# Kernel tuning notes

Hardware: AMD Instinct MI355X
Metric: run time of the kernel (lower is better)

Reference implementation:

```python
import math
import jax, jax.numpy as jnp
import numpy as np

SQ = 5  # locality window width (static, from init_kwargs)

def _locality_mask_np(hidden_size: int, width: int) -> np.ndarray:
    """[H, H] 0/1 mask: units live on a side x side grid; unit i connects to
    unit j iff their circular (wrap-around) Chebyshev grid distance <= width//2.
    mask_type='circular' -> toroidal wrap."""
    side = int(round(math.sqrt(hidden_size)))
    assert side * side == hidden_size
    r = np.arange(hidden_size) // side
    c = np.arange(hidden_size) % side
    dr = np.abs(r[:, None] - r[None, :])
    dc = np.abs(c[:, None] - c[None, :])
    dr = np.minimum(dr, side - dr)  # circular wrap
    dc = np.minimum(dc, side - dc)
    half = width // 2
    return ((dr <= half) & (dc <= half)).astype(np.float32)


def setup_inputs() -> dict:
    key = jax.random.key(0)
    ks = jax.random.split(key, 8)
    B, S, H = 8, 2048, 1024
    scale = 0.02
    x = jax.random.normal(ks[0], (B, S, H), dtype=jnp.float32)
    Wq = jax.random.normal(ks[1], (H, H), dtype=jnp.float32) * scale
    Wk = jax.random.normal(ks[2], (H, H), dtype=jnp.float32) * scale
    Wv = jax.random.normal(ks[3], (H, H), dtype=jnp.float32) * scale
    bq = jnp.zeros((H,), dtype=jnp.float32)
    bk = jnp.zeros((H,), dtype=jnp.float32)
    bv = jnp.zeros((H,), dtype=jnp.float32)
    Wl = jax.random.normal(ks[4], (H, H), dtype=jnp.float32) * scale
    return {"x": x, "Wq": Wq, "bq": bq, "Wk": Wk, "bk": bk,
            "Wv": Wv, "bv": bv, "Wl": Wl}


def reference(x, Wq, bq, Wk, bk, Wv, bv, Wl):
    H = x.shape[-1]
    mask = jnp.asarray(_locality_mask_np(H, SQ))  # [H, H], static
    # Locally-connected q/k/v projections: dense weight elementwise-masked.
    q = x @ (Wq * mask).T + bq  # [B, S, H]
    k = x @ (Wk * mask).T + bk
    v = x @ (Wv * mask).T + bv
    # Learned spatial querying: locality-masked learned map applied to query.
    q = q @ (Wl * mask).T  # [B, S, H]
    # Manual attention (dropout is identity in eval / p=0).
    scores = jnp.einsum("bsh,bth->bst", q, k) / math.sqrt(H)  # [B, S, S]
    probs = jax.nn.softmax(scores, axis=-1)
    out = jnp.einsum("bst,bth->bsh", probs, v)  # [B, S, H]
    return out, probs
```

## Files before the change

kernel.cpp:

```cpp
#include <hip/hip_runtime.h>

typedef __attribute__((ext_vector_type(8))) short short8;
typedef __attribute__((ext_vector_type(4))) float floatx4;

__device__ __forceinline__ unsigned short f2bf(float f) {
  union { float f; unsigned int u; } x; x.f = f;
  unsigned int r = (x.u + 0x7fffu + ((x.u >> 16) & 1u)) >> 16;
  return (unsigned short)r;
}
__device__ __forceinline__ float bf2f(unsigned short u) {
  union { unsigned int u; float f; } x; x.u = ((unsigned int)u) << 16;
  return x.f;
}

__device__ __forceinline__ void gload_lds16(const void* g, void* l) {
  __builtin_amdgcn_global_load_lds((const __attribute__((address_space(1))) void*)g,
                                   (__attribute__((address_space(3))) void*)l,
                                   16, 0, 0);
}

__global__ __launch_bounds__(128) void prep_weights(
    const float* __restrict__ Wq, const float* __restrict__ Wk,
    const float* __restrict__ Wv, const float* __restrict__ Wl,
    const float* __restrict__ bq, const float* __restrict__ bk,
    const float* __restrict__ bv,
    unsigned short* __restrict__ Wqkv, float* __restrict__ biasAll) {
  const int i = blockIdx.x;
  const int r = i >> 5, c = i & 31;
  const int t = threadIdx.x;
  {
    short8 z = (short8){0, 0, 0, 0, 0, 0, 0, 0};
    ((short8*)Wqkv)[i * 128 + t] = z;
    ((short8*)Wqkv)[(1024 + i) * 128 + t] = z;
    ((short8*)Wqkv)[(2048 + i) * 128 + t] = z;
  }
  __syncthreads();
  if (t < 25) {
    int dr = t / 5 - 2, dc = t % 5 - 2;
    int j = (((r + dr) & 31) << 5) | ((c + dc) & 31);
    Wqkv[(1024 + i) * 1024 + j] = f2bf(Wk[i * 1024 + j]);
    Wqkv[(2048 + i) * 1024 + j] = f2bf(Wv[i * 1024 + j]);
  }
  if (t < 81) {
    int dr = t / 9 - 4, dc = t % 9 - 4;
    int j = (((r + dr) & 31) << 5) | ((c + dc) & 31);
    float s = 0.f;
    int erlo = dr - 2 < -2 ? -2 : dr - 2, erhi = dr + 2 > 2 ? 2 : dr + 2;
    int eclo = dc - 2 < -2 ? -2 : dc - 2, echi = dc + 2 > 2 ? 2 : dc + 2;
    for (int er = erlo; er <= erhi; ++er)
      for (int ec = eclo; ec <= echi; ++ec) {
        int m = (((r + er) & 31) << 5) | ((c + ec) & 31);
        s += Wl[i * 1024 + m] * Wq[m * 1024 + j];
      }
    Wqkv[i * 1024 + j] = f2bf(s);
  }
  if (t == 96) {
    float s = 0.f;
    for (int e = 0; e < 25; ++e) {
      int dr = e / 5 - 2, dc = e % 5 - 2;
      int m = (((r + dr) & 31) << 5) | ((c + dc) & 31);
      s += Wl[i * 1024 + m] * bq[m];
    }
    biasAll[i] = s;
  }
  if (t == 97) biasAll[1024 + i] = bk[i];
  if (t == 98) biasAll[2048 + i] = bv[i];
}

__global__ __launch_bounds__(256) void cast_bf16(const float4* __restrict__ x,
                                                 ushort4* __restrict__ xb) {
  int i = blockIdx.x * 256 + threadIdx.x;
  float4 v = x[i];
  ushort4 o;
  o.x = f2bf(v.x); o.y = f2bf(v.y); o.z = f2bf(v.z); o.w = f2bf(v.w);
  xb[i] = o;
}

template <int OUTMODE>
__global__ __launch_bounds__(512, 2) void gemm256(
    const unsigned short* __restrict__ A, const unsigned short* __restrict__ B,
    void* __restrict__ Cv, const float* __restrict__ auxc, float* __restrict__ auxw,
    int lda, int ldb, int ldc, int K, float scale,
    size_t sA, size_t sB, size_t sC, int nx, int ny) {
  __shared__ __align__(16) unsigned short lds[67584];
  const int t = threadIdx.x;
  const int lane = t & 63;
  const int wv = t >> 6;
  const int wm = wv >> 2;
  const int wn = wv & 3;
  const int l15 = lane & 15, lq = lane >> 4;

  const int nwg = gridDim.x;
  const int hid = blockIdx.x;
  const int logical = (hid & 7) * (nwg >> 3) + (hid >> 3);
  const int bn = logical % nx;
  const int bm = (logical / nx) % ny;
  const int bz = logical / (nx * ny);

  A += sA * bz; B += sB * bz;

  const int srow = t >> 3;
  const int sg = (t & 7) ^ (srow & 7);

#define STG_A(h, tile_) do {                                                     \
    gload_lds16(A + (size_t)(bm * 256 + (h) * 128 + srow) * lda + (tile_) * 64 + sg * 8, \
                &lds[(((tile_) & 1) << 14) + (h) * 8192 + wv * 512]);            \
    gload_lds16(A + (size_t)(bm * 256 + (h) * 128 + 64 + srow) * lda + (tile_) * 64 + sg * 8, \
                &lds[(((tile_) & 1) << 14) + (h) * 8192 + 4096 + wv * 512]);     \
  } while (0)
#define STG_B(h, tile_) do {                                                     \
    gload_lds16(B + (size_t)(bn * 256 + (h) * 128 + srow) * ldb + (tile_) * 64 + sg * 8, \
                &lds[32768 + (((tile_) & 1) << 14) + (h) * 8192 + wv * 512]);    \
    gload_lds16(B + (size_t)(bn * 256 + (h) * 128 + 64 + srow) * ldb + (tile_) * 64 + sg * 8, \
                &lds[32768 + (((tile_) & 1) << 14) + (h) * 8192 + 4096 + wv * 512]); \
  } while (0)

#define LOADA(arr, ro)                                                           \
  _Pragma("unroll") for (int i = 0; i < 4; ++i) {                                \
    int rA = wm * 128 + (ro) + i * 16 + l15;                                     \
    _Pragma("unroll") for (int ks = 0; ks < 2; ++ks)                             \
      arr[i][ks] = *(const short8*)&lds[bo_ + rA * 64 + (((ks * 4 + lq) ^ (rA & 7)) << 3)]; \
  }
#define LOADB(arr, ro)                                                           \
  _Pragma("unroll") for (int j = 0; j < 2; ++j) {                                \
    int rB = wn * 64 + (ro) + j * 16 + l15;                                      \
    _Pragma("unroll") for (int ks = 0; ks < 2; ++ks)                             \
      arr[j][ks] = *(const short8*)&lds[32768 + bo_ + rB * 64 + (((ks * 4 + lq) ^ (rB & 7)) << 3)]; \
  }
#define MFMA8(mb, nb, aa, bb)                                                    \
  _Pragma("unroll") for (int i = 0; i < 4; ++i)                                  \
    _Pragma("unroll") for (int j = 0; j < 2; ++j) {                              \
      acc[(mb) + i][(nb) + j] = __builtin_amdgcn_mfma_f32_16x16x32_bf16(         \
          aa[i][0], bb[j][0], acc[(mb) + i][(nb) + j], 0, 0, 0);                 \
      acc[(mb) + i][(nb) + j] = __builtin_amdgcn_mfma_f32_16x16x32_bf16(         \
          aa[i][1], bb[j][1], acc[(mb) + i][(nb) + j], 0, 0, 0);                 \
    }
#define FENCE asm volatile("" ::: "memory")
#define BAR __builtin_amdgcn_s_barrier()
#define SP1 __builtin_amdgcn_s_setprio(1)
#define SP0 __builtin_amdgcn_s_setprio(0)

  floatx4 acc[8][4];
#pragma unroll
  for (int i = 0; i < 8; ++i)
#pragma unroll
    for (int j = 0; j < 4; ++j) acc[i][j] = (floatx4){0.f, 0.f, 0.f, 0.f};

  const int NT = K >> 6;

  STG_A(0, 0); STG_A(1, 0); STG_B(0, 0); STG_B(1, 0);
  FENCE;
  STG_B(0, 1); STG_A(0, 1); STG_B(1, 1);
  asm volatile("s_waitcnt vmcnt(6)" ::: "memory");
  BAR;

  for (int T = 0; T < NT; T += 2) {
    short8 aF[4][2], bFa[2][2], bFb[2][2];
    {
      const int bo_ = 0;
      LOADA(aF, 0); LOADB(bFa, 0);
      STG_A(1, T + 1);
      FENCE; BAR;
      SP1; MFMA8(0, 0, aF, bFa); SP0;
      FENCE; BAR;
      LOADB(bFb, 32);
      FENCE; BAR;
      SP1; MFMA8(0, 2, aF, bFb); SP0;
      FENCE; BAR;
      LOADA(aF, 64);
      if (T + 2 < NT) STG_B(0, T + 2);
      FENCE; BAR;
      SP1; MFMA8(4, 2, aF, bFb); SP0;
      FENCE; BAR;
      if (T + 2 < NT) STG_A(0, T + 2);
      FENCE; BAR;
      SP1; MFMA8(4, 0, aF, bFa); SP0;
      if (T + 2 < NT) { asm volatile("s_waitcnt vmcnt(4)" ::: "memory"); }
      else            { asm volatile("s_waitcnt vmcnt(0)" ::: "memory"); }
      FENCE; BAR;
    }
    {
      const int bo_ = 1 << 14;
      LOADA(aF, 0); LOADB(bFa, 0);
      if (T + 2 < NT) { STG_B(1, T + 2); STG_A(1, T + 2); }
      FENCE; BAR;
      SP1; MFMA8(0, 0, aF, bFa); SP0;
      FENCE; BAR;
      LOADB(bFb, 32);
      FENCE; BAR;
      SP1; MFMA8(0, 2, aF, bFb); SP0;
      FENCE; BAR;
      LOADA(aF, 64);
      if (T + 3 < NT) STG_B(0, T + 3);
      FENCE; BAR;
      SP1; MFMA8(4, 2, aF, bFb); SP0;
      FENCE; BAR;
      if (T + 3 < NT) { STG_A(0, T + 3); STG_B(1, T + 3); }
      FENCE; BAR;
      SP1; MFMA8(4, 0, aF, bFa); SP0;
      if (T + 3 < NT) { asm volatile("s_waitcnt vmcnt(6)" ::: "memory"); }
      else            { asm volatile("s_waitcnt vmcnt(0)" ::: "memory"); }
      FENCE; BAR;
    }
  }
#undef STG_A
#undef STG_B
#undef LOADA
#undef LOADB
#undef MFMA8

  const int row0 = bm * 256 + wm * 128;
  const int col0 = bn * 256 + wn * 64;

  if (OUTMODE == 0) {
    if (bn < 8) {
      unsigned short* C = (unsigned short*)Cv;
#pragma unroll
      for (int m = 0; m < 8; ++m) {
        int rb = row0 + ((m >> 2) << 6) + ((m & 3) << 4) + (lq << 2);
#pragma unroll
        for (int n = 0; n < 4; ++n) {
          int col = col0 + ((n >> 1) << 5) + ((n & 1) << 4) + l15;
          float bb = auxc[col];
#pragma unroll
          for (int r2 = 0; r2 < 4; ++r2)
            C[(size_t)(rb + r2) * ldc + col] = f2bf(acc[m][n][r2] + bb);
        }
      }
    } else {
      unsigned short (*lds2)[264] = (unsigned short (*)[264])lds;
#pragma unroll
      for (int m = 0; m < 8; ++m) {
        int sr = wm * 128 + ((m >> 2) << 6) + ((m & 3) << 4) + (lq << 2);
#pragma unroll
        for (int n = 0; n < 4; ++n) {
          int colg = col0 + ((n >> 1) << 5) + ((n & 1) << 4) + l15;
          int h = (colg - 2048) & 255;
          float bb = auxc[colg];
          ushort4 pk;
          pk.x = f2bf(acc[m][n][0] + bb);
          pk.y = f2bf(acc[m][n][1] + bb);
          pk.z = f2bf(acc[m][n][2] + bb);
          pk.w = f2bf(acc[m][n][3] + bb);
          *(ushort4*)&lds2[h][sr] = pk;
        }
      }
      __syncthreads();
      unsigned short* vTp = (unsigned short*)auxw;
      const int b = bm >> 3;
      const int s0 = (bm & 7) * 256;
      const int h0 = (bn - 8) * 256;
      const int hh = t >> 1, sh = (t & 1) * 128;
      unsigned short* dst = vTp + ((size_t)b * 1024 + h0 + hh) * 2048 + s0 + sh;
      const unsigned short* src = &lds2[hh][sh];
#pragma unroll
      for (int k2 = 0; k2 < 16; ++k2)
        *(short8*)&dst[k2 * 8] = *(const short8*)&src[k2 * 8];
    }
  } else if (OUTMODE == 2) {
    unsigned short* C = (unsigned short*)Cv + sC * bz;
    float p[8][4];
#pragma unroll
    for (int m = 0; m < 8; ++m)
#pragma unroll
      for (int r2 = 0; r2 < 4; ++r2) p[m][r2] = 0.f;
#pragma unroll
    for (int m = 0; m < 8; ++m) {
      int rb = row0 + ((m >> 2) << 6) + ((m & 3) << 4) + (lq << 2);
#pragma unroll
      for (int n = 0; n < 4; ++n) {
        int col = col0 + ((n >> 1) << 5) + ((n & 1) << 4) + l15;
#pragma unroll
        for (int r2 = 0; r2 < 4; ++r2) {
          float e = __expf(acc[m][n][r2] * scale);
          C[(size_t)(rb + r2) * ldc + col] = f2bf(e);
          p[m][r2] += e;
        }
      }
    }
#pragma unroll
    for (int m = 0; m < 8; ++m)
#pragma unroll
      for (int r2 = 0; r2 < 4; ++r2) {
        float v = p[m][r2];
        v += __shfl_xor(v, 1); v += __shfl_xor(v, 2);
        v += __shfl_xor(v, 4); v += __shfl_xor(v, 8);
        p[m][r2] = v;
      }
    float* sred = (float*)lds;
    if (l15 == 0) {
#pragma unroll
      for (int m = 0; m < 8; ++m)
#pragma unroll
        for (int r2 = 0; r2 < 4; ++r2)
          sred[wn * 256 + wm * 128 + ((m >> 2) << 6) + ((m & 3) << 4) + (lq << 2) + r2] = p[m][r2];
    }
    __syncthreads();
    if (t < 256) {
      float L = sred[t] + sred[256 + t] + sred[512 + t] + sred[768 + t];
      auxw[((size_t)bz * 2048 + bm * 256 + t) * 8 + bn] = L;
    }
  } else {
    float* C = (float*)Cv + sC * bz;
#pragma unroll
    for (int m = 0; m < 8; ++m) {
      int rb = row0 + ((m >> 2) << 6) + ((m & 3) << 4) + (lq << 2);
      float il[4];
#pragma unroll
      for (int r2 = 0; r2 < 4; ++r2)
        il[r2] = auxc[(size_t)bz * 2048 + rb + r2];
#pragma unroll
      for (int n = 0; n < 4; ++n) {
        int col = col0 + ((n >> 1) << 5) + ((n & 1) << 4) + l15;
#pragma unroll
        for (int r2 = 0; r2 < 4; ++r2)
          C[(size_t)(rb + r2) * ldc + col] = acc[m][n][r2] * il[r2];
      }
    }
  }
}

__global__ __launch_bounds__(256) void finish_softmax(
    const float* __restrict__ Lpart, const unsigned short* __restrict__ pb,
    float* __restrict__ invL, float* __restrict__ probs) {
  const size_t row = blockIdx.x;
  const int t = threadIdx.x;
  __shared__ float sInv;
  if (t < 64) {
    float s = (t < 8) ? Lpart[row * 8 + t] : 0.f;
    s += __shfl_xor(s, 1); s += __shfl_xor(s, 2); s += __shfl_xor(s, 4);
    if (t == 0) {
      float inv = 1.0f / s;
      sInv = inv;
      invL[row] = inv;
    }
  }
  __syncthreads();
  float inv = sInv;
  const ushort4* pv = (const ushort4*)(pb + row * 2048);
  float4* pr = (float4*)(probs + row * 2048);
  ushort4 a = pv[t * 2], b = pv[t * 2 + 1];
  float4 o0, o1;
  o0.x = bf2f(a.x) * inv; o0.y = bf2f(a.y) * inv;
  o0.z = bf2f(a.z) * inv; o0.w = bf2f(a.w) * inv;
  o1.x = bf2f(b.x) * inv; o1.y = bf2f(b.y) * inv;
  o1.z = bf2f(b.z) * inv; o1.w = bf2f(b.w) * inv;
  pr[t * 2] = o0; pr[t * 2 + 1] = o1;
}

extern "C" void kernel_launch(void* const* d_in, const int* in_sizes, int n_in,
                              void* d_out, int out_size, void* d_ws, size_t ws_size,
                              hipStream_t stream) {
  const float* x  = (const float*)d_in[0];
  const float* Wq = (const float*)d_in[1];
  const float* bq = (const float*)d_in[2];
  const float* Wk = (const float*)d_in[3];
  const float* bk = (const float*)d_in[4];
  const float* Wv = (const float*)d_in[5];
  const float* bv = (const float*)d_in[6];
  const float* Wl = (const float*)d_in[7];

  const int B = 8, S = 2048, H = 1024;
  float* out   = (float*)d_out;
  float* probs = (float*)d_out + (size_t)B * S * H;

  char* ws = (char*)d_ws;
  unsigned short* qkv  = (unsigned short*)(ws + 0);
  unsigned short* pb   = (unsigned short*)(ws + 100663296);
  unsigned short* xb   = (unsigned short*)(ws + 167772160);
  unsigned short* vT   = (unsigned short*)(ws + 167772160);
  unsigned short* Wqkv = (unsigned short*)(ws + 201326592);
  float* biasAll       = (float*)(ws + 207618048);
  float* Lpart         = (float*)(ws + 207630336);
  float* invL          = (float*)(ws + 208678912);
  vT = (unsigned short*)(ws + 209715200);

  prep_weights<<<1024, 128, 0, stream>>>(Wq, Wk, Wv, Wl, bq, bk, bv, Wqkv, biasAll);
  cast_bf16<<<16384, 256, 0, stream>>>((const float4*)x, (ushort4*)xb);

  gemm256<0><<<768, 512, 0, stream>>>(xb, Wqkv, qkv, biasAll, (float*)vT,
      H, H, 3 * H, H, 1.f, 0, 0, 0, 12, 64);

  gemm256<2><<<512, 512, 0, stream>>>(qkv, qkv + 1024, pb, nullptr, Lpart,
      3 * H, 3 * H, S, H, 1.0f / 32.0f, (size_t)S * 3 * H, (size_t)S * 3 * H, (size_t)S * S, 8, 8);

  finish_softmax<<<16384, 256, 0, stream>>>(Lpart, pb, invL, probs);

  gemm256<3><<<256, 512, 0, stream>>>(pb, vT, out, invL, nullptr,
      S, S, H, S, 1.0f, (size_t)S * S, (size_t)H * S, (size_t)S * H, 4, 8);
}
```

Baseline: 526.2 us.

## Fuse softmax normalization and probs write into PV GEMM; merge prep and cast

Removes the finish_softmax kernel. The PV GEMM now sums the partial row sums into inverse normalizers kept in LDS. It also writes the fp32 probs tile from the bf16 P tiles already staged in LDS, but only in the column-block tiles that match its bn, so each P element is written once. It also merges the weight prep and x cast kernels into one launch. This avoids re-reading the bf16 probs from global memory and saves two launches, but adds global stores and LDS reads inside the GEMM main loop, which may disturb the MFMA schedule.

```diff
diff --git a/kernel.cpp b/kernel.cpp
--- a/kernel.cpp
+++ b/kernel.cpp
@@ -19,15 +19,27 @@
                                    16, 0, 0);
 }
 
-__global__ __launch_bounds__(128) void prep_weights(
+__global__ __launch_bounds__(128) void prep_cast(
     const float* __restrict__ Wq, const float* __restrict__ Wk,
     const float* __restrict__ Wv, const float* __restrict__ Wl,
     const float* __restrict__ bq, const float* __restrict__ bk,
     const float* __restrict__ bv,
-    unsigned short* __restrict__ Wqkv, float* __restrict__ biasAll) {
-  const int i = blockIdx.x;
+    unsigned short* __restrict__ Wqkv, float* __restrict__ biasAll,
+    const float4* __restrict__ x, ushort4* __restrict__ xb) {
+  const int t = threadIdx.x;
+  if (blockIdx.x < 16384) {
+    int i = blockIdx.x * 256 + t;
+#pragma unroll
+    for (int k = 0; k < 2; ++k) {
+      float4 v = x[i + k * 128];
+      ushort4 o;
+      o.x = f2bf(v.x); o.y = f2bf(v.y); o.z = f2bf(v.z); o.w = f2bf(v.w);
+      xb[i + k * 128] = o;
+    }
+    return;
+  }
+  const int i = blockIdx.x - 16384;
   const int r = i >> 5, c = i & 31;
-  const int t = threadIdx.x;
   {
     short8 z = (short8){0, 0, 0, 0, 0, 0, 0, 0};
     ((short8*)Wqkv)[i * 128 + t] = z;
@@ -65,15 +77,6 @@
   }
   if (t == 97) biasAll[1024 + i] = bk[i];
   if (t == 98) biasAll[2048 + i] = bv[i];
-}
-
-__global__ __launch_bounds__(256) void cast_bf16(const float4* __restrict__ x,
-                                                 ushort4* __restrict__ xb) {
-  int i = blockIdx.x * 256 + threadIdx.x;
-  float4 v = x[i];
-  ushort4 o;
-  o.x = f2bf(v.x); o.y = f2bf(v.y); o.z = f2bf(v.z); o.w = f2bf(v.w);
-  xb[i] = o;
 }
 
 template <int OUTMODE>
@@ -102,6 +105,23 @@
   const int srow = t >> 3;
   const int sg = (t & 7) ^ (srow & 7);
 
+  float* lds_invL = (float*)&lds[65536];
+  float* probs_base = (OUTMODE == 3) ? (auxw + (size_t)bz * 4194304) : nullptr;
+  float il_h0 = 0.f, il_h1 = 0.f;
+
+  if (OUTMODE == 3) {
+    if (t < 256) {
+      const float4* Lp = (const float4*)&auxc[((size_t)bz * 2048 + bm * 256 + t) * 8];
+      float4 a = Lp[0], b = Lp[1];
+      float s = a.x + a.y + a.z + a.w + b.x + b.y + b.z + b.w;
+      lds_invL[t] = 1.0f / s;
+    }
+    asm volatile("s_waitcnt vmcnt(0) lgkmcnt(0)" ::: "memory");
+    __builtin_amdgcn_s_barrier();
+    il_h0 = lds_invL[t >> 2];
+    il_h1 = lds_invL[128 + (t >> 2)];
+  }
+
 #define STG_A(h, tile_) do {                                                     \
     gload_lds16(A + (size_t)(bm * 256 + (h) * 128 + srow) * lda + (tile_) * 64 + sg * 8, \
                 &lds[(((tile_) & 1) << 14) + (h) * 8192 + wv * 512]);            \
@@ -135,6 +155,26 @@
       acc[(mb) + i][(nb) + j] = __builtin_amdgcn_mfma_f32_16x16x32_bf16(         \
           aa[i][1], bb[j][1], acc[(mb) + i][(nb) + j], 0, 0, 0);                 \
     }
+#define PWRITE(bo_, T_, hb, il) do {                                             \
+    int pr = (hb) + (t >> 2);                                                    \
+    int g0 = (t & 3) * 2;                                                        \
+    short8 e0 = *(const short8*)&lds[(bo_) + pr * 64 + (((g0 ^ (pr & 7))) << 3)];\
+    short8 e1 = *(const short8*)&lds[(bo_) + pr * 64 + ((((g0 + 1) ^ (pr & 7))) << 3)]; \
+    float* dst = probs_base + (size_t)(bm * 256 + pr) * 2048 + (T_) * 64 + (t & 3) * 16; \
+    float4 w;                                                                    \
+    w.x = bf2f((unsigned short)e0[0]) * (il); w.y = bf2f((unsigned short)e0[1]) * (il); \
+    w.z = bf2f((unsigned short)e0[2]) * (il); w.w = bf2f((unsigned short)e0[3]) * (il); \
+    *(float4*)&dst[0] = w;                                                       \
+    w.x = bf2f((unsigned short)e0[4]) * (il); w.y = bf2f((unsigned short)e0[5]) * (il); \
+    w.z = bf2f((unsigned short)e0[6]) * (il); w.w = bf2f((unsigned short)e0[7]) * (il); \
+    *(float4*)&dst[4] = w;                                                       \
+    w.x = bf2f((unsigned short)e1[0]) * (il); w.y = bf2f((unsigned short)e1[1]) * (il); \
+    w.z = bf2f((unsigned short)e1[2]) * (il); w.w = bf2f((unsigned short)e1[3]) * (il); \
+    *(float4*)&dst[8] = w;                                                       \
+    w.x = bf2f((unsigned short)e1[4]) * (il); w.y = bf2f((unsigned short)e1[5]) * (il); \
+    w.z = bf2f((unsigned short)e1[6]) * (il); w.w = bf2f((unsigned short)e1[7]) * (il); \
+    *(float4*)&dst[12] = w;                                                      \
+  } while (0)
 #define FENCE asm volatile("" ::: "memory")
 #define BAR __builtin_amdgcn_s_barrier()
 #define SP1 __builtin_amdgcn_s_setprio(1)
@@ -156,10 +196,13 @@
 
   for (int T = 0; T < NT; T += 2) {
     short8 aF[4][2], bFa[2][2], bFb[2][2];
+    const bool pw0 = (OUTMODE == 3) && (T >= bn * 8) && (T < bn * 8 + 8);
+    const bool pw1 = (OUTMODE == 3) && (T + 1 >= bn * 8) && (T + 1 < bn * 8 + 8);
     {
       const int bo_ = 0;
       LOADA(aF, 0); LOADB(bFa, 0);
       STG_A(1, T + 1);
+      if (pw0) PWRITE(bo_, T, 0, il_h0);
       FENCE; BAR;
       SP1; MFMA8(0, 0, aF, bFa); SP0;
       FENCE; BAR;
@@ -169,6 +212,7 @@
       FENCE; BAR;
       LOADA(aF, 64);
       if (T + 2 < NT) STG_B(0, T + 2);
+      if (pw0) PWRITE(bo_, T, 128, il_h1);
       FENCE; BAR;
       SP1; MFMA8(4, 2, aF, bFb); SP0;
       FENCE; BAR;
@@ -183,6 +227,7 @@
       const int bo_ = 1 << 14;
       LOADA(aF, 0); LOADB(bFa, 0);
       if (T + 2 < NT) { STG_B(1, T + 2); STG_A(1, T + 2); }
+      if (pw1) PWRITE(bo_, T + 1, 0, il_h0);
       FENCE; BAR;
       SP1; MFMA8(0, 0, aF, bFa); SP0;
       FENCE; BAR;
@@ -192,6 +237,7 @@
       FENCE; BAR;
       LOADA(aF, 64);
       if (T + 3 < NT) STG_B(0, T + 3);
+      if (pw1) PWRITE(bo_, T + 1, 128, il_h1);
       FENCE; BAR;
       SP1; MFMA8(4, 2, aF, bFb); SP0;
       FENCE; BAR;
@@ -208,6 +254,7 @@
 #undef LOADA
 #undef LOADB
 #undef MFMA8
+#undef PWRITE
 
   const int row0 = bm * 256 + wm * 128;
   const int col0 = bn * 256 + wn * 64;
@@ -304,48 +351,19 @@
     float* C = (float*)Cv + sC * bz;
 #pragma unroll
     for (int m = 0; m < 8; ++m) {
+      int lr = wm * 128 + ((m >> 2) << 6) + ((m & 3) << 4) + (lq << 2);
+      float4 il4 = *(const float4*)&lds_invL[lr];
       int rb = row0 + ((m >> 2) << 6) + ((m & 3) << 4) + (lq << 2);
-      float il[4];
-#pragma unroll
-      for (int r2 = 0; r2 < 4; ++r2)
-        il[r2] = auxc[(size_t)bz * 2048 + rb + r2];
 #pragma unroll
       for (int n = 0; n < 4; ++n) {
         int col = col0 + ((n >> 1) << 5) + ((n & 1) << 4) + l15;
-#pragma unroll
-        for (int r2 = 0; r2 < 4; ++r2)
-          C[(size_t)(rb + r2) * ldc + col] = acc[m][n][r2] * il[r2];
-      }
-    }
-  }
-}
-
-__global__ __launch_bounds__(256) void finish_softmax(
-    const float* __restrict__ Lpart, const unsigned short* __restrict__ pb,
-    float* __restrict__ invL, float* __restrict__ probs) {
-  const size_t row = blockIdx.x;
-  const int t = threadIdx.x;
-  __shared__ float sInv;
-  if (t < 64) {
-    float s = (t < 8) ? Lpart[row * 8 + t] : 0.f;
-    s += __shfl_xor(s, 1); s += __shfl_xor(s, 2); s += __shfl_xor(s, 4);
-    if (t == 0) {
-      float inv = 1.0f / s;
-      sInv = inv;
-      invL[row] = inv;
-    }
-  }
-  __syncthreads();
-  float inv = sInv;
-  const ushort4* pv = (const ushort4*)(pb + row * 2048);
-  float4* pr = (float4*)(probs + row * 2048);
-  ushort4 a = pv[t * 2], b = pv[t * 2 + 1];
-  float4 o0, o1;
-  o0.x = bf2f(a.x) * inv; o0.y = bf2f(a.y) * inv;
-  o0.z = bf2f(a.z) * inv; o0.w = bf2f(a.w) * inv;
-  o1.x = bf2f(b.x) * inv; o1.y = bf2f(b.y) * inv;
-  o1.z = bf2f(b.z) * inv; o1.w = bf2f(b.w) * inv;
-  pr[t * 2] = o0; pr[t * 2 + 1] = o1;
+        C[(size_t)(rb + 0) * ldc + col] = acc[m][n][0] * il4.x;
+        C[(size_t)(rb + 1) * ldc + col] = acc[m][n][1] * il4.y;
+        C[(size_t)(rb + 2) * ldc + col] = acc[m][n][2] * il4.z;
+        C[(size_t)(rb + 3) * ldc + col] = acc[m][n][3] * il4.w;
+      }
+    }
+  }
 }
 
 extern "C" void kernel_launch(void* const* d_in, const int* in_sizes, int n_in,
@@ -368,15 +386,13 @@
   unsigned short* qkv  = (unsigned short*)(ws + 0);
   unsigned short* pb   = (unsigned short*)(ws + 100663296);
   unsigned short* xb   = (unsigned short*)(ws + 167772160);
-  unsigned short* vT   = (unsigned short*)(ws + 167772160);
   unsigned short* Wqkv = (unsigned short*)(ws + 201326592);
   float* biasAll       = (float*)(ws + 207618048);
   float* Lpart         = (float*)(ws + 207630336);
-  float* invL          = (float*)(ws + 208678912);
-  vT = (unsigned short*)(ws + 209715200);
-
-  prep_weights<<<1024, 128, 0, stream>>>(Wq, Wk, Wv, Wl, bq, bk, bv, Wqkv, biasAll);
-  cast_bf16<<<16384, 256, 0, stream>>>((const float4*)x, (ushort4*)xb);
+  unsigned short* vT   = (unsigned short*)(ws + 209715200);
+
+  prep_cast<<<17408, 128, 0, stream>>>(Wq, Wk, Wv, Wl, bq, bk, bv, Wqkv, biasAll,
+                                       (const float4*)x, (ushort4*)xb);
 
   gemm256<0><<<768, 512, 0, stream>>>(xb, Wqkv, qkv, biasAll, (float*)vT,
       H, H, 3 * H, H, 1.f, 0, 0, 0, 12, 64);
@@ -384,8 +400,6 @@
   gemm256<2><<<512, 512, 0, stream>>>(qkv, qkv + 1024, pb, nullptr, Lpart,
       3 * H, 3 * H, S, H, 1.0f / 32.0f, (size_t)S * 3 * H, (size_t)S * 3 * H, (size_t)S * S, 8, 8);
 
-  finish_softmax<<<16384, 256, 0, stream>>>(Lpart, pb, invL, probs);
-
-  gemm256<3><<<256, 512, 0, stream>>>(pb, vT, out, invL, nullptr,
+  gemm256<3><<<256, 512, 0, stream>>>(pb, vT, out, Lpart, probs,
       S, S, H, S, 1.0f, (size_t)S * S, (size_t)H * S, (size_t)S * H, 4, 8);
 }
```

After: 554.9 us. +5.4%, slower.
